# Performance work log

Measured on AMD Instinct MI355X. Metric: run time of the kernel, lower is better.

The kernel has to match this reference:

```python
import jax, jax.numpy as jnp
import numpy as np

B, T, S, H, V = 4, 512, 1024, 768, 50257

def setup_inputs() -> dict:
    key = jax.random.key(0)
    k1, k2, k3, k4, k5, k6 = jax.random.split(key, 6)
    input_ids_to_copy = jax.random.randint(k1, (B, S), 0, V)
    cross_attentions = jax.random.uniform(k2, (B, T, S), dtype=jnp.float32)
    # normalize like attention weights
    cross_attentions = cross_attentions / jnp.sum(cross_attentions, axis=-1, keepdims=True)
    src_hidden_states = jax.random.normal(k3, (B, S, H), dtype=jnp.float32)
    tgt_hidden_states = jax.random.normal(k4, (B, T, H), dtype=jnp.float32)
    # p_gen_head = Linear(2H, 1) + Sigmoid
    W_pgen = jax.random.normal(k5, (2 * H, 1), dtype=jnp.float32) * (1.0 / np.sqrt(2 * H))
    b_pgen = jnp.zeros((1,), dtype=jnp.float32)
    return {
        "input_ids_to_copy": input_ids_to_copy,
        "cross_attentions": cross_attentions,
        "src_hidden_states": src_hidden_states,
        "tgt_hidden_states": tgt_hidden_states,
        "W_pgen": W_pgen,
        "b_pgen": b_pgen,
    }

def _copy_logits(attn_bts, ids_bs, vocab_size):
    # logits[b,t,v] = sum_s attn[b,t,s] * (ids[b,s] == v)
    # Efficient scatter-add over source positions instead of one-hot + matmul.
    def per_batch(attn_ts, ids_s):
        # attn_ts: [T,S], ids_s: [S] -> segment_sum over S -> [V,T] -> [T,V]
        return jax.ops.segment_sum(attn_ts.T, ids_s, num_segments=vocab_size).T
    return jax.vmap(per_batch)(attn_bts, ids_bs)

def reference(input_ids_to_copy, cross_attentions, src_hidden_states,
              tgt_hidden_states, W_pgen, b_pgen):
    # context_vectors: [B,T,H]
    context_vectors = jnp.einsum('bts,bsh->bth', cross_attentions, src_hidden_states)
    total_states = jnp.concatenate((context_vectors, tgt_hidden_states), axis=-1)  # [B,T,2H]
    p_gen = jax.nn.sigmoid(total_states @ W_pgen + b_pgen)  # [B,T,1]
    logits = _copy_logits(cross_attentions, input_ids_to_copy, V)  # [B,T,V]
    return (p_gen, logits)
```

## Files before the change

### kernel.cpp

```cpp
#include <hip/hip_runtime.h>
#include <hip/hip_bf16.h>
#include <math.h>

#define BB 4
#define TT 512
#define SS 1024
#define HH 768
#define VV 50257

__global__ __launch_bounds__(256) void proj_kernel(
    const float* __restrict__ src,
    const float* __restrict__ tgt,
    const float* __restrict__ W,
    const float* __restrict__ bptr,
    float* __restrict__ src_proj,
    float* __restrict__ tgt_proj)
{
    const int wave = threadIdx.x >> 6;
    const int lane = threadIdx.x & 63;
    const int row  = blockIdx.x * 4 + wave;

    const float* vec;
    const float* w;
    if (row < BB * SS) {
        vec = src + (size_t)row * HH;
        w   = W;
    } else {
        vec = tgt + (size_t)(row - BB * SS) * HH;
        w   = W + HH;
    }
    const float4* v4 = (const float4*)vec;
    const float4* w4 = (const float4*)w;

    float acc = 0.f;
#pragma unroll
    for (int k = 0; k < 3; ++k) {
        float4 a = v4[k * 64 + lane];
        float4 b = w4[k * 64 + lane];
        acc += a.x * b.x + a.y * b.y + a.z * b.z + a.w * b.w;
    }
#pragma unroll
    for (int off = 32; off > 0; off >>= 1) acc += __shfl_down(acc, off);

    if (lane == 0) {
        if (row < BB * SS) src_proj[row] = acc;
        else               tgt_proj[row - BB * SS] = acc + bptr[0];
    }
}

__global__ __launch_bounds__(256) void row_kernel(
    const int*   __restrict__ ids,
    const float* __restrict__ attn,
    const float* __restrict__ src_proj,
    const float* __restrict__ tgt_proj,
    float* __restrict__ out)
{
    const int row = blockIdx.x;
    const int b   = row >> 9;
    const int tid = threadIdx.x;

    float* logits = out + (BB * TT) + (size_t)row * VV;

    uintptr_t addr = (uintptr_t)logits;
    int head = (int)(((16u - (addr & 15u)) & 15u) >> 2);
    if (tid < head) logits[tid] = 0.f;
    const int n4 = (VV - head) >> 2;
    float4* p4 = (float4*)(logits + head);
    const float4 z4 = make_float4(0.f, 0.f, 0.f, 0.f);
    for (int i = tid; i < n4; i += 256) p4[i] = z4;
    const int done = head + (n4 << 2);
    for (int i = done + tid; i < VV; i += 256) logits[i] = 0.f;

    __syncthreads();

    const float* attn_row = attn + (size_t)row * SS;
    const int*   ids_b    = ids + b * SS;
    const float* sp_b     = src_proj + b * SS;

    float acc = 0.f;
#pragma unroll
    for (int k = 0; k < SS / 256; ++k) {
        const int s = tid + k * 256;
        const float a = attn_row[s];
        const int   id = ids_b[s];
        atomicAdd(logits + id, a);
        acc += a * sp_b[s];
    }

#pragma unroll
    for (int off = 32; off > 0; off >>= 1) acc += __shfl_down(acc, off);
    __shared__ float wsum[4];
    if ((tid & 63) == 0) wsum[tid >> 6] = acc;
    __syncthreads();
    if (tid == 0) {
        const float sum = wsum[0] + wsum[1] + wsum[2] + wsum[3];
        const float x = sum + tgt_proj[row];
        out[row] = 1.f / (1.f + expf(-x));
    }
}

extern "C" void kernel_launch(void* const* d_in, const int* in_sizes, int n_in,
                              void* d_out, int out_size, void* d_ws, size_t ws_size,
                              hipStream_t stream) {
    const int*   ids  = (const int*)d_in[0];
    const float* attn = (const float*)d_in[1];
    const float* src  = (const float*)d_in[2];
    const float* tgt  = (const float*)d_in[3];
    const float* W    = (const float*)d_in[4];
    const float* bp   = (const float*)d_in[5];

    float* out = (float*)d_out;
    float* ws  = (float*)d_ws;
    float* src_proj = ws;
    float* tgt_proj = ws + BB * SS;

    proj_kernel<<<(BB * SS + BB * TT) / 4, 256, 0, stream>>>(
        src, tgt, W, bp, src_proj, tgt_proj);

    row_kernel<<<BB * TT, 256, 0, stream>>>(ids, attn, src_proj, tgt_proj, out);
}
```

Measured before the change: 518.3 us.

## Build per-batch vocab bitmap and rank table to scatter in LDS, write logits once

Adds a per-batch setup kernel that builds a bitmap of the vocabulary ids present in each batch's source, a prefix-count table over its words, and a compact rank for each source position. The row kernel now accumulates attention into a small shared-memory array indexed by rank, then writes each logits row once, filling values through a bitmap lookup. This replaces the zero-fill, barrier and global atomics that touched the same logits row again. It costs an extra small launch and some LDS and popcount work per output float4.

```diff
diff --git a/kernel.cpp b/kernel.cpp
--- a/kernel.cpp
+++ b/kernel.cpp
@@ -7,14 +7,12 @@
 #define SS 1024
 #define HH 768
 #define VV 50257
+#define NW 1571
 
 __global__ __launch_bounds__(256) void proj_kernel(
-    const float* __restrict__ src,
-    const float* __restrict__ tgt,
-    const float* __restrict__ W,
-    const float* __restrict__ bptr,
-    float* __restrict__ src_proj,
-    float* __restrict__ tgt_proj)
+    const float* __restrict__ src, const float* __restrict__ tgt,
+    const float* __restrict__ W, const float* __restrict__ bptr,
+    float* __restrict__ src_proj, float* __restrict__ tgt_proj)
 {
     const int wave = threadIdx.x >> 6;
     const int lane = threadIdx.x & 63;
@@ -22,13 +20,8 @@
 
     const float* vec;
     const float* w;
-    if (row < BB * SS) {
-        vec = src + (size_t)row * HH;
-        w   = W;
-    } else {
-        vec = tgt + (size_t)(row - BB * SS) * HH;
-        w   = W + HH;
-    }
+    if (row < BB * SS) { vec = src + (size_t)row * HH;            w = W; }
+    else               { vec = tgt + (size_t)(row - BB*SS) * HH;  w = W + HH; }
     const float4* v4 = (const float4*)vec;
     const float4* w4 = (const float4*)w;
 
@@ -41,62 +34,153 @@
     }
 #pragma unroll
     for (int off = 32; off > 0; off >>= 1) acc += __shfl_down(acc, off);
-
     if (lane == 0) {
         if (row < BB * SS) src_proj[row] = acc;
         else               tgt_proj[row - BB * SS] = acc + bptr[0];
     }
 }
 
+__global__ __launch_bounds__(256) void batch_setup(
+    const int* __restrict__ ids,
+    unsigned* __restrict__ bm_g,
+    unsigned* __restrict__ pre_g,
+    unsigned short* __restrict__ rank_g)
+{
+    __shared__ unsigned bm[NW];
+    __shared__ unsigned pre[NW];
+    __shared__ unsigned scan[256];
+    const int b = blockIdx.x, tid = threadIdx.x;
+
+    for (int i = tid; i < NW; i += 256) bm[i] = 0u;
+    __syncthreads();
+    const int* idb = ids + b * SS;
+    for (int s = tid; s < SS; s += 256) {
+        const int v = idb[s];
+        atomicOr(&bm[v >> 5], 1u << (v & 31));
+    }
+    __syncthreads();
+
+    unsigned cnt[7];
+    unsigned local = 0;
+    const int w0 = tid * 7;
+#pragma unroll
+    for (int k = 0; k < 7; ++k) {
+        const int w = w0 + k;
+        cnt[k] = local;
+        local += (w < NW) ? (unsigned)__popc(bm[w]) : 0u;
+    }
+    scan[tid] = local;
+    __syncthreads();
+    for (int off = 1; off < 256; off <<= 1) {
+        const unsigned mine = scan[tid];
+        const unsigned add  = (tid >= off) ? scan[tid - off] : 0u;
+        __syncthreads();
+        scan[tid] = mine + add;
+        __syncthreads();
+    }
+    const unsigned excl = (tid > 0) ? scan[tid - 1] : 0u;
+#pragma unroll
+    for (int k = 0; k < 7; ++k) {
+        const int w = w0 + k;
+        if (w < NW) {
+            const unsigned p = excl + cnt[k];
+            pre[w] = p;
+            pre_g[b * NW + w] = p;
+            bm_g[b * NW + w]  = bm[w];
+        }
+    }
+    __syncthreads();
+    for (int s = tid; s < SS; s += 256) {
+        const int v = idb[s];
+        const unsigned w = (unsigned)v >> 5, bit = (unsigned)v & 31u;
+        const unsigned r = pre[w] + (unsigned)__popc(bm[w] & ((1u << bit) - 1u));
+        rank_g[b * SS + s] = (unsigned short)r;
+    }
+}
+
+__device__ __forceinline__ float lut1(int v, const unsigned* bm,
+                                      const unsigned* pre, const float* vals)
+{
+    const unsigned w = bm[v >> 5];
+    const unsigned bit = (unsigned)v & 31u;
+    if ((w >> bit) & 1u)
+        return vals[pre[v >> 5] + (unsigned)__popc(w & ((1u << bit) - 1u))];
+    return 0.f;
+}
+
 __global__ __launch_bounds__(256) void row_kernel(
-    const int*   __restrict__ ids,
     const float* __restrict__ attn,
     const float* __restrict__ src_proj,
     const float* __restrict__ tgt_proj,
+    const unsigned* __restrict__ bm_g,
+    const unsigned* __restrict__ pre_g,
+    const unsigned short* __restrict__ rank_g,
     float* __restrict__ out)
 {
+    __shared__ unsigned bm[NW];
+    __shared__ unsigned pre[NW];
+    __shared__ unsigned short rnk[SS];
+    __shared__ float vals[SS];
+    __shared__ float wsum[4];
+
     const int row = blockIdx.x;
     const int b   = row >> 9;
     const int tid = threadIdx.x;
 
+    for (int i = tid; i < NW; i += 256) { bm[i] = bm_g[b*NW+i]; pre[i] = pre_g[b*NW+i]; }
+    for (int i = tid; i < SS; i += 256) rnk[i] = rank_g[b*SS+i];
+    for (int i = tid; i < SS; i += 256) vals[i] = 0.f;
+    __syncthreads();
+
+    const float* arow = attn + (size_t)row * SS;
+    const float* spb  = src_proj + b * SS;
+    float acc = 0.f;
+#pragma unroll
+    for (int k = 0; k < SS / 256; ++k) {
+        const int s = tid + k * 256;
+        const float a = arow[s];
+        atomicAdd(&vals[rnk[s]], a);
+        acc += a * spb[s];
+    }
+#pragma unroll
+    for (int off = 32; off > 0; off >>= 1) acc += __shfl_down(acc, off);
+    if ((tid & 63) == 0) wsum[tid >> 6] = acc;
+    __syncthreads();
+    if (tid == 0) {
+        const float x = wsum[0] + wsum[1] + wsum[2] + wsum[3] + tgt_proj[row];
+        out[row] = 1.f / (1.f + expf(-x));
+    }
+
     float* logits = out + (BB * TT) + (size_t)row * VV;
-
-    uintptr_t addr = (uintptr_t)logits;
-    int head = (int)(((16u - (addr & 15u)) & 15u) >> 2);
-    if (tid < head) logits[tid] = 0.f;
+    const uintptr_t addr = (uintptr_t)logits;
+    const int head = (int)(((16u - (unsigned)(addr & 15u)) & 15u) >> 2);
+    if (tid < head) logits[tid] = lut1(tid, bm, pre, vals);
+
     const int n4 = (VV - head) >> 2;
     float4* p4 = (float4*)(logits + head);
-    const float4 z4 = make_float4(0.f, 0.f, 0.f, 0.f);
-    for (int i = tid; i < n4; i += 256) p4[i] = z4;
+    for (int i = tid; i < n4; i += 256) {
+        const int v0 = head + (i << 2);
+        float4 o = make_float4(0.f, 0.f, 0.f, 0.f);
+        const unsigned w  = bm[v0 >> 5];
+        const unsigned sh = (unsigned)v0 & 31u;
+        unsigned nib;
+        if (sh <= 28u) {
+            nib = (w >> sh) & 0xFu;
+        } else {
+            const unsigned hi = bm[(v0 >> 5) + 1];
+            nib = ((w >> sh) | (hi << (32u - sh))) & 0xFu;
+        }
+        if (nib) {
+            o.x = lut1(v0,     bm, pre, vals);
+            o.y = lut1(v0 + 1, bm, pre, vals);
+            o.z = lut1(v0 + 2, bm, pre, vals);
+            o.w = lut1(v0 + 3, bm, pre, vals);
+        }
+        p4[i] = o;
+    }
     const int done = head + (n4 << 2);
-    for (int i = done + tid; i < VV; i += 256) logits[i] = 0.f;
-
-    __syncthreads();
-
-    const float* attn_row = attn + (size_t)row * SS;
-    const int*   ids_b    = ids + b * SS;
-    const float* sp_b     = src_proj + b * SS;
-
-    float acc = 0.f;
-#pragma unroll
-    for (int k = 0; k < SS / 256; ++k) {
-        const int s = tid + k * 256;
-        const float a = attn_row[s];
-        const int   id = ids_b[s];
-        atomicAdd(logits + id, a);
-        acc += a * sp_b[s];
-    }
-
-#pragma unroll
-    for (int off = 32; off > 0; off >>= 1) acc += __shfl_down(acc, off);
-    __shared__ float wsum[4];
-    if ((tid & 63) == 0) wsum[tid >> 6] = acc;
-    __syncthreads();
-    if (tid == 0) {
-        const float sum = wsum[0] + wsum[1] + wsum[2] + wsum[3];
-        const float x = sum + tgt_proj[row];
-        out[row] = 1.f / (1.f + expf(-x));
-    }
+    for (int v = done + tid; v < VV; v += 256)
+        logits[v] = lut1(v, bm, pre, vals);
 }
 
 extern "C" void kernel_launch(void* const* d_in, const int* in_sizes, int n_in,
@@ -110,12 +194,17 @@
     const float* bp   = (const float*)d_in[5];
 
     float* out = (float*)d_out;
-    float* ws  = (float*)d_ws;
-    float* src_proj = ws;
-    float* tgt_proj = ws + BB * SS;
+
+    char* wsb = (char*)d_ws;
+    float*          src_proj = (float*)wsb;
+    float*          tgt_proj = src_proj + BB * SS;
+    unsigned*       bm_g     = (unsigned*)(tgt_proj + BB * TT);
+    unsigned*       pre_g    = bm_g + BB * NW;
+    unsigned short* rank_g   = (unsigned short*)(pre_g + BB * NW);
 
     proj_kernel<<<(BB * SS + BB * TT) / 4, 256, 0, stream>>>(
         src, tgt, W, bp, src_proj, tgt_proj);
-
-    row_kernel<<<BB * TT, 256, 0, stream>>>(ids, attn, src_proj, tgt_proj, out);
-}
+    batch_setup<<<BB, 256, 0, stream>>>(ids, bm_g, pre_g, rank_g);
+    row_kernel<<<BB * TT, 256, 0, stream>>>(
+        attn, src_proj, tgt_proj, bm_g, pre_g, rank_g, out);
+}
```

Result: faster. 466.6 us (-10.0%).
